# Performance work log

Measured on AMD Instinct MI355X. Metric: run time of the kernel, lower is better.

## Reference

```python
import jax, jax.numpy as jnp
import numpy as np
import math

B, C, H, W = 4, 64, 64, 64
N_HEAD = 1
GROUPS = 16
EPS = 1e-5


def dwconv_block(x, w, b, pad):
    # ReflectionPad2d(pad) -> depthwise Conv2d -> LeakyReLU(0.01)
    xp = jnp.pad(x, ((0, 0), (0, 0), (pad, pad), (pad, pad)), mode='reflect')
    y = jax.lax.conv_general_dilated(
        xp, w, window_strides=(1, 1), padding='VALID',
        dimension_numbers=('NCHW', 'OIHW', 'NCHW'),
        feature_group_count=x.shape[1])
    y = y + b[None, :, None, None]
    return jax.nn.leaky_relu(y, 0.01)


def group_norm(x, w, b):
    bb, c, h, ww = x.shape
    xg = x.reshape(bb, GROUPS, c // GROUPS, h, ww)
    mu = xg.mean(axis=(2, 3, 4), keepdims=True)
    var = xg.var(axis=(2, 3, 4), keepdims=True)
    xg = (xg - mu) * jax.lax.rsqrt(var + EPS)
    return xg.reshape(bb, c, h, ww) * w[None, :, None, None] + b[None, :, None, None]


def attention(q, k, v):
    # q,k,v: [B, n_head, head_dim, H, W]; softmax over flattened key grid
    bb, n, d, h, ww = q.shape
    qf = q.reshape(bb, n, d, h * ww)
    kf = k.reshape(bb, n, d, h * ww)
    vf = v.reshape(bb, n, d, h * ww)
    scores = jnp.einsum('bndq,bndk->bnqk', qf, kf) / math.sqrt(C)
    attn = jax.nn.softmax(scores, axis=-1)  # [B,n,HW,HW]
    out = jnp.einsum('bnqk,bndk->bndq', attn, vf)
    return out.reshape(bb, n * d, h, ww)


def conv1x1(x, w, b=None):
    y = jnp.einsum('oc,bchw->bohw', w, x)
    if b is not None:
        y = y + b[None, :, None, None]
    return y


def setup_inputs() -> dict:
    key = jax.random.key(0)
    ks = jax.random.split(key, 16)
    s = lambda fan: 1.0 / math.sqrt(fan)
    return {
        'inputs': jax.random.normal(ks[0], (B, C, H, W), jnp.float32),
        'dw1_w': jax.random.normal(ks[1], (C, 1, 3, 3), jnp.float32) * s(9),
        'dw1_b': jnp.zeros((C,), jnp.float32),
        'dw2_w': jax.random.normal(ks[2], (C, 1, 5, 5), jnp.float32) * s(25),
        'dw2_b': jnp.zeros((C,), jnp.float32),
        'gnA_w': jnp.ones((C,), jnp.float32),
        'gnA_b': jnp.zeros((C,), jnp.float32),
        'gnB_w': jnp.ones((C,), jnp.float32),
        'gnB_b': jnp.zeros((C,), jnp.float32),
        'qkvA_w': jax.random.normal(ks[3], (3 * C, C), jnp.float32) * s(C),
        'qkvB_w': jax.random.normal(ks[4], (3 * C, C), jnp.float32) * s(C),
        'outA_w': jax.random.normal(ks[5], (C, C), jnp.float32) * s(C),
        'outA_b': jnp.zeros((C,), jnp.float32),
        'outB_w': jax.random.normal(ks[6], (C, C), jnp.float32) * s(C),
        'outB_b': jnp.zeros((C,), jnp.float32),
    }


def reference(inputs, dw1_w, dw1_b, dw2_w, dw2_b, gnA_w, gnA_b, gnB_w, gnB_b,
              qkvA_w, qkvB_w, outA_w, outA_b, outB_w, outB_b):
    x = dwconv_block(inputs, dw1_w, dw1_b, pad=1)
    y = dwconv_block(inputs, dw2_w, dw2_b, pad=2)
    head_dim = C // N_HEAD

    x_A = group_norm(x, gnA_w, gnA_b)
    qkv_A = conv1x1(x_A, qkvA_w).reshape(B, N_HEAD, head_dim * 3, H, W)
    qA, kA, vA = jnp.split(qkv_A, 3, axis=2)

    x_B = group_norm(y, gnB_w, gnB_b)
    qkv_B = conv1x1(x_B, qkvB_w).reshape(B, N_HEAD, head_dim * 3, H, W)
    qB, kB, vB = jnp.split(qkv_B, 3, axis=2)

    # branch A: queries from B, keys/values from A
    out_A = conv1x1(attention(qB, kA, vA), outA_w, outA_b) + x_A
    # branch B: queries from A, keys/values from B
    out_B = conv1x1(attention(qA, kB, vB), outB_w, outB_b) + x_B
    return jnp.concatenate((out_A, out_B), axis=1)
```

## Files before the change

### kernel.cpp

```cpp
#include <hip/hip_runtime.h>
#include <hip/hip_bf16.h>

#define HW 4096
#define CCH 64

typedef __attribute__((ext_vector_type(8))) short short8;
typedef __attribute__((ext_vector_type(4))) float f32x4;
typedef unsigned short ushort_t;
typedef unsigned long long u64;

#define SCALE_Q 0.18033688f

__device__ __forceinline__ unsigned short f2b(float f) {
  unsigned u = __float_as_uint(f);
  return (unsigned short)((u + 0x7fff + ((u >> 16) & 1)) >> 16);
}
__device__ __forceinline__ float b2f(ushort_t u) {
  return __uint_as_float(((unsigned)u) << 16);
}
__device__ __forceinline__ unsigned cvtpk(float lo, float hi) {
  unsigned r;
  asm volatile("v_cvt_pk_bf16_f32 %0, %1, %2" : "=v"(r) : "v"(lo), "v"(hi));
  return r;
}
__device__ __forceinline__ void gload16(const void* g, void* l) {
  __builtin_amdgcn_global_load_lds(
      (const __attribute__((address_space(1))) unsigned int*)g,
      (__attribute__((address_space(3))) unsigned int*)l, 16, 0, 0);
}

__global__ void __launch_bounds__(256) k_dwconv(
    const float* __restrict__ in, const float* __restrict__ w1, const float* __restrict__ b1,
    const float* __restrict__ w2, const float* __restrict__ b2,
    ushort_t* __restrict__ x, ushort_t* __restrict__ y, float* __restrict__ sums) {
  __shared__ float sm[20 * 68];
  __shared__ float red[4][4];
  const int bc = blockIdx.x >> 2;
  const int r0 = (blockIdx.x & 3) * 16;
  const int c = bc & 63;
  const float* p = in + bc * HW;
  const int tid = threadIdx.x;
  for (int idx = tid; idx < 20 * 68; idx += 256) {
    int r = r0 + idx / 68 - 2, cc = idx % 68 - 2;
    r = r < 0 ? -r : (r > 63 ? 126 - r : r);
    cc = cc < 0 ? -cc : (cc > 63 ? 126 - cc : cc);
    sm[idx] = p[r * 64 + cc];
  }
  float w1r[9], w2r[25];
  for (int i = 0; i < 9; i++) w1r[i] = w1[c * 9 + i];
  for (int i = 0; i < 25; i++) w2r[i] = w2[c * 25 + i];
  const float bb1 = b1[c], bb2 = b2[c];
  __syncthreads();

  const int i = tid >> 4;
  const int j0 = (tid & 15) * 4;
  float rv[5][8];
  for (int u = 0; u < 5; u++) {
    *(f32x4*)&rv[u][0] = *(const f32x4*)&sm[(i + u) * 68 + j0];
    *(f32x4*)&rv[u][4] = *(const f32x4*)&sm[(i + u) * 68 + j0 + 4];
  }
  float a1[4], a2[4];
  for (int px = 0; px < 4; px++) {
    float s2 = bb2;
    for (int u = 0; u < 5; u++)
      for (int v = 0; v < 5; v++) s2 += w2r[u * 5 + v] * rv[u][px + v];
    float s1 = bb1;
    for (int u = 0; u < 3; u++)
      for (int v = 0; v < 3; v++) s1 += w1r[u * 3 + v] * rv[u + 1][px + 1 + v];
    a1[px] = s1 > 0.f ? s1 : 0.01f * s1;
    a2[px] = s2 > 0.f ? s2 : 0.01f * s2;
  }
  ushort_t t1[4], t2[4];
  for (int px = 0; px < 4; px++) { t1[px] = f2b(a1[px]); t2[px] = f2b(a2[px]); }
  const int off = bc * HW + (r0 + i) * 64 + j0;
  *(u64*)(x + off) = *(const u64*)t1;
  *(u64*)(y + off) = *(const u64*)t2;

  float s1 = 0, q1 = 0, s2 = 0, q2 = 0;
  for (int px = 0; px < 4; px++) {
    s1 += a1[px]; q1 += a1[px] * a1[px];
    s2 += a2[px]; q2 += a2[px] * a2[px];
  }
  for (int o = 1; o < 64; o <<= 1) {
    s1 += __shfl_xor(s1, o); q1 += __shfl_xor(q1, o);
    s2 += __shfl_xor(s2, o); q2 += __shfl_xor(q2, o);
  }
  if ((tid & 63) == 0) {
    red[tid >> 6][0] = s1; red[tid >> 6][1] = q1;
    red[tid >> 6][2] = s2; red[tid >> 6][3] = q2;
  }
  __syncthreads();
  if (tid == 0) {
    float r4[4];
    for (int k = 0; k < 4; k++)
      r4[k] = red[0][k] + red[1][k] + red[2][k] + red[3][k];
    const int b = bc >> 6, g = (bc & 63) >> 2;
    const int base = b * 32 + g * 2;
    atomicAdd(&sums[base], r4[0]);       atomicAdd(&sums[base + 1], r4[1]);
    atomicAdd(&sums[128 + base], r4[2]); atomicAdd(&sums[128 + base + 1], r4[3]);
  }
}

__global__ void __launch_bounds__(256) k_qkv(
    const ushort_t* __restrict__ xbf, const ushort_t* __restrict__ ybf,
    const float* __restrict__ sums,
    const float* __restrict__ gwA, const float* __restrict__ gbA,
    const float* __restrict__ gwB, const float* __restrict__ gbB,
    const float* __restrict__ wA, const float* __restrict__ wB,
    ushort_t* __restrict__ Qt, ushort_t* __restrict__ Kt, ushort_t* __restrict__ Vv) {
  __shared__ float scs[64], shs[64];
  const int id = blockIdx.x * 256 + threadIdx.x;
  const int pg = id & 1023;
  const int chunk = (id >> 10) % 24;
  const int h = id / (1024 * 24);
  const int b = h >> 1, br = h & 1;
  if (threadIdx.x < 64) {
    const int ch = threadIdx.x, g = ch >> 2;
    const float s = sums[br * 128 + b * 32 + g * 2];
    const float ss = sums[br * 128 + b * 32 + g * 2 + 1];
    const float mu = s * (1.f / 16384.f);
    const float var = ss * (1.f / 16384.f) - mu * mu;
    const float rsig = rsqrtf(var + 1e-5f);
    const float a = rsig * (br ? gwB : gwA)[ch];
    scs[ch] = a;
    shs[ch] = (br ? gbB : gbA)[ch] - mu * a;
  }
  __syncthreads();
  const ushort_t* X = (br ? ybf : xbf) + b * (CCH * HW);
  const float* W = br ? wB : wA;
  const int pix0 = pg * 4;
  const int r0 = chunk * 8;
  float acc[8][4];
  for (int r = 0; r < 8; r++) for (int p = 0; p < 4; p++) acc[r][p] = 0.f;
  for (int cc = 0; cc < 64; cc++) {
    const float sc = scs[cc], sh = shs[cc];
    const u64 raw = *(const u64*)(X + cc * HW + pix0);
    f32x4 xv;
    for (int p = 0; p < 4; p++)
      xv[p] = b2f((ushort_t)(raw >> (16 * p))) * sc + sh;
    for (int r = 0; r < 8; r++) {
      float wv = W[(r0 + r) * 64 + cc];
      for (int p = 0; p < 4; p++) acc[r][p] += wv * xv[p];
    }
  }
  if (chunk < 16) {
    ushort_t* dst = chunk < 8 ? Qt : Kt;
    const float qs = chunk < 8 ? SCALE_Q : 1.0f;
    const int d0 = (chunk & 7) * 8;
    for (int p = 0; p < 4; p++) {
      short8 v;
      for (int r = 0; r < 8; r++) v[r] = (short)f2b(acc[r][p] * qs);
      *(short8*)(dst + ((h * HW + pix0 + p) << 6) + d0) = v;
    }
  } else {
    const int d0 = (chunk - 16) * 8;
    for (int r = 0; r < 8; r++) {
      ushort_t tmp[4];
      for (int p = 0; p < 4; p++) tmp[p] = f2b(acc[r][p]);
      *(u64*)(Vv + (h * CCH + d0 + r) * HW + pix0) = *(const u64*)tmp;
    }
  }
}

__global__ void __launch_bounds__(256, 2) k_attn(
    const ushort_t* __restrict__ Qt, const ushort_t* __restrict__ Kt,
    const ushort_t* __restrict__ Vv,
    const float* __restrict__ oAw, const float* __restrict__ oAb,
    const float* __restrict__ oBw, const float* __restrict__ oBb,
    const ushort_t* __restrict__ xbf, const ushort_t* __restrict__ ybf,
    const float* __restrict__ sums,
    const float* __restrict__ gwA, const float* __restrict__ gbA,
    const float* __restrict__ gwB, const float* __restrict__ gbB,
    float* __restrict__ out) {
  __shared__ __align__(16) char lds[74240];
  const int h = blockIdx.x >> 6;
  const int qt = blockIdx.x & 63;
  const int b = h >> 1, br = h & 1;
  const int qh = b * 2 + (1 - br);
  const int tid = threadIdx.x;
  const int lane = tid & 63;
  const int wave = tid >> 6;
  const int q = lane & 15, g = lane >> 4;
  const int qbase = qt * 64 + wave * 16;

  float* scs = (float*)(lds + 73728);
  float* shs = scs + 64;
  if (tid < 64) {
    const int ch = tid, gg = ch >> 2;
    const float s = sums[br * 128 + b * 32 + gg * 2];
    const float ss = sums[br * 128 + b * 32 + gg * 2 + 1];
    const float mu = s * (1.f / 16384.f);
    const float var = ss * (1.f / 16384.f) - mu * mu;
    const float rsig = rsqrtf(var + 1e-5f);
    const float a = rsig * (br ? gwB : gwA)[ch];
    scs[ch] = a;
    shs[ch] = (br ? gbB : gbA)[ch] - mu * a;
  }

  const ushort_t* Qp = Qt + ((qh * HW + qbase + q) << 6);
  const short8 qf0 = *(const short8*)(Qp + g * 8);
  const short8 qf1 = *(const short8*)(Qp + 32 + g * 8);

  const ushort_t* Kh = Kt + ((u64)h * HW << 6);
  const ushort_t* Vh = Vv + (u64)h * (CCH * HW);
  const ushort_t* gk[4];
  const ushort_t* gv[4];
  for (int j = 0; j < 4; j++) {
    const int idx = j * 256 + tid;
    const int rK = idx >> 3, cK = (idx & 7) ^ (rK & 7);
    gk[j] = Kh + (rK << 6) + (cK << 3);
    const int rV = idx >> 4, cV = (idx & 15) ^ (rV & 7);
    gv[j] = Vh + rV * HW + (cV << 3);
  }
  char* lK = lds + (tid << 4);
  char* lV = lds + 16384 + (tid << 4);

  float m_run = -1e30f;
  f32x4 o[4] = {};
  f32x4 accl = {};
  char* wp = lds + 65536 + wave * 2048 + (q << 7);
  const int sw = (q & 7) << 4;
  short8 ones;
  for (int j = 0; j < 8; j++) ones[j] = (short)0x3F80;

  for (int j = 0; j < 4; j++) gload16(gk[j], lK + j * 4096);
  for (int j = 0; j < 4; j++) gload16(gv[j], lV + j * 4096);

#pragma unroll 1
  for (int it = 0; it < 32; ++it) {
    if (it < 31) {
      const int nb = (it + 1) & 1;
      for (int j = 0; j < 4; j++) gload16(gk[j] + (it + 1) * 8192, lK + nb * 32768 + j * 4096);
      for (int j = 0; j < 4; j++) gload16(gv[j] + (it + 1) * 128, lV + nb * 32768 + j * 4096);
      asm volatile("s_waitcnt vmcnt(8)" ::: "memory");
    } else {
      asm volatile("s_waitcnt vmcnt(0)" ::: "memory");
    }
    __builtin_amdgcn_s_barrier();

    const char* kb = lds + (it & 1) * 32768;
    const char* vb = kb + 16384;
#pragma unroll
    for (int ph = 0; ph < 2; ph++) {
      short8 ka[4][2], va[4][2];
      for (int c = 0; c < 4; c++)
        for (int s = 0; s < 2; s++)
          ka[c][s] = *(const short8*)(kb + ((ph * 64 + c * 16 + q) << 7) +
                                      (((s * 4 + g) ^ (q & 7)) << 4));
      for (int cd = 0; cd < 4; cd++)
        for (int s = 0; s < 2; s++)
          va[cd][s] = *(const short8*)(vb + ((cd * 16 + q) << 8) +
                                       (((ph * 8 + s * 4 + g) ^ (q & 7)) << 4));

      f32x4 sa[4];
      for (int c = 0; c < 4; c++) {
        f32x4 zz = {0.f, 0.f, 0.f, 0.f};
        zz = __builtin_amdgcn_mfma_f32_16x16x32_bf16(ka[c][0], qf0, zz, 0, 0, 0);
        sa[c] = __builtin_amdgcn_mfma_f32_16x16x32_bf16(ka[c][1], qf1, zz, 0, 0, 0);
      }
      float m0 = fmaxf(fmaxf(fmaxf(sa[0][0], sa[0][1]), sa[0][2]), sa[0][3]);
      float m1 = fmaxf(fmaxf(fmaxf(sa[1][0], sa[1][1]), sa[1][2]), sa[1][3]);
      float m2 = fmaxf(fmaxf(fmaxf(sa[2][0], sa[2][1]), sa[2][2]), sa[2][3]);
      float m3 = fmaxf(fmaxf(fmaxf(sa[3][0], sa[3][1]), sa[3][2]), sa[3][3]);
      float mloc = fmaxf(fmaxf(m0, m1), fmaxf(m2, m3));
      mloc = fmaxf(mloc, __shfl_xor(mloc, 16));
      mloc = fmaxf(mloc, __shfl_xor(mloc, 32));
      if (!__all(mloc <= m_run + 8.f)) {
        const float mnew = fmaxf(m_run, mloc);
        const float alpha = exp2f(m_run - mnew);
        for (int cd = 0; cd < 4; cd++)
          for (int i = 0; i < 4; i++) o[cd][i] *= alpha;
        for (int i = 0; i < 4; i++) accl[i] *= alpha;
        m_run = mnew;
      }
      u64 pk[4];
      for (int c = 0; c < 4; c++) {
        float p0 = exp2f(sa[c][0] - m_run), p1 = exp2f(sa[c][1] - m_run);
        float p2 = exp2f(sa[c][2] - m_run), p3 = exp2f(sa[c][3] - m_run);
        pk[c] = (u64)cvtpk(p0, p1) | ((u64)cvtpk(p2, p3) << 32);
      }
      for (int c = 0; c < 4; c++)
        *(u64*)(wp + (((c << 5) | (g << 3)) ^ sw)) = pk[c];
      asm volatile("s_waitcnt lgkmcnt(0)" ::: "memory");
      __builtin_amdgcn_sched_barrier(0);
      const short8 pb0 = *(const short8*)(wp + ((g << 4) ^ sw));
      const short8 pb1 = *(const short8*)(wp + ((64 | (g << 4)) ^ sw));
      for (int cd = 0; cd < 4; cd++) {
        o[cd] = __builtin_amdgcn_mfma_f32_16x16x32_bf16(va[cd][0], pb0, o[cd], 0, 0, 0);
        o[cd] = __builtin_amdgcn_mfma_f32_16x16x32_bf16(va[cd][1], pb1, o[cd], 0, 0, 0);
      }
      accl = __builtin_amdgcn_mfma_f32_16x16x32_bf16(ones, pb0, accl, 0, 0, 0);
      accl = __builtin_amdgcn_mfma_f32_16x16x32_bf16(ones, pb1, accl, 0, 0, 0);
    }
    __builtin_amdgcn_s_barrier();
  }

  __syncthreads();
  float* smW = (float*)(lds + wave * 4096);
  const float inv = 1.f / accl[0];
  for (int cd = 0; cd < 4; cd++) {
    f32x4 v;
    for (int i = 0; i < 4; i++) v[i] = o[cd][i] * inv;
    *(f32x4*)(smW + q * 64 + (((cd * 4 + g) ^ q) << 2)) = v;
  }
  asm volatile("s_waitcnt lgkmcnt(0)" ::: "memory");
  __builtin_amdgcn_sched_barrier(0);

  const float* W    = br ? oBw : oAw;
  const float* bias = br ? oBb : oAb;
  const ushort_t* xR = (br ? ybf : xbf) + b * (CCH * HW);
  const int q2 = lane & 15, g2 = lane >> 4;
  const float* smR = (float*)(lds + wave * 4096) + q2 * 64;
  const int pix = qt * 64 + wave * 16 + q2;

  float acc[16];
  for (int oi = 0; oi < 16; oi++) acc[oi] = bias[g2 * 16 + oi];
  for (int c4 = 0; c4 < 16; c4++) {
    const f32x4 Lv = *(const f32x4*)(smR + ((c4 ^ q2) << 2));
    for (int oi = 0; oi < 16; oi++) {
      const f32x4 wv = *(const f32x4*)(W + (g2 * 16 + oi) * 64 + c4 * 4);
      acc[oi] += wv[0] * Lv[0] + wv[1] * Lv[1] + wv[2] * Lv[2] + wv[3] * Lv[3];
    }
  }
  for (int oi = 0; oi < 16; oi++) {
    const int ch = g2 * 16 + oi;
    const float xn = b2f(xR[ch * HW + pix]) * scs[ch] + shs[ch];
    out[(b * 128 + br * 64 + ch) * HW + pix] = acc[oi] + xn;
  }
}

extern "C" void kernel_launch(void* const* d_in, const int* in_sizes, int n_in,
                              void* d_out, int out_size, void* d_ws, size_t ws_size,
                              hipStream_t stream) {
  const float* in   = (const float*)d_in[0];
  const float* dw1w = (const float*)d_in[1];
  const float* dw1b = (const float*)d_in[2];
  const float* dw2w = (const float*)d_in[3];
  const float* dw2b = (const float*)d_in[4];
  const float* gnAw = (const float*)d_in[5];
  const float* gnAb = (const float*)d_in[6];
  const float* gnBw = (const float*)d_in[7];
  const float* gnBb = (const float*)d_in[8];
  const float* qAw  = (const float*)d_in[9];
  const float* qBw  = (const float*)d_in[10];
  const float* oAw  = (const float*)d_in[11];
  const float* oAb  = (const float*)d_in[12];
  const float* oBw  = (const float*)d_in[13];
  const float* oBb  = (const float*)d_in[14];
  float* out = (float*)d_out;

  char* ws = (char*)d_ws;
  ushort_t* xbf = (ushort_t*)ws;
  ushort_t* ybf = xbf + 1048576;
  ushort_t* Qt  = ybf + 1048576;
  ushort_t* Kt  = Qt + 2097152;
  ushort_t* Vv  = Kt + 2097152;
  float* sums   = (float*)(Vv + 2097152);

  hipMemsetAsync(sums, 0, 256 * sizeof(float), stream);
  k_dwconv<<<1024, 256, 0, stream>>>(in, dw1w, dw1b, dw2w, dw2b, xbf, ybf, sums);
  k_qkv<<<768, 256, 0, stream>>>(xbf, ybf, sums, gnAw, gnAb, gnBw, gnBb,
                                 qAw, qBw, Qt, Kt, Vv);
  k_attn<<<512, 256, 0, stream>>>(Qt, Kt, Vv, oAw, oAb, oBw, oBb,
                                  xbf, ybf, sums, gnAw, gnAb, gnBw, gnBb, out);
}
```

Measured before the change: 224.7 us.

## Halve attention KV tile for 3 blocks/CU and drop atomic GN stats memset

The attention kernel's K/V tile shrinks from 128 to 64 keys per iteration, which halves the double-buffered LDS footprint and raises launch bounds to allow three blocks per CU. The inner loop runs 64 iterations with one phase each instead of 32 with two. Group-norm partial sums are now written per (channel, strip) with plain stores instead of atomics, and reduced with shuffles in the consumers, which removes the hipMemsetAsync launch. The trade-off is more barriers and loop overhead per key processed, plus register pressure under the tighter launch bound.

Result: faster. 219.8 us (-2.2%).

```diff
diff --git a/kernel.cpp b/kernel.cpp
--- a/kernel.cpp
+++ b/kernel.cpp
@@ -36,7 +36,8 @@
   __shared__ float sm[20 * 68];
   __shared__ float red[4][4];
   const int bc = blockIdx.x >> 2;
-  const int r0 = (blockIdx.x & 3) * 16;
+  const int strip = blockIdx.x & 3;
+  const int r0 = strip * 16;
   const int c = bc & 63;
   const float* p = in + bc * HW;
   const int tid = threadIdx.x;
@@ -94,11 +95,30 @@
     float r4[4];
     for (int k = 0; k < 4; k++)
       r4[k] = red[0][k] + red[1][k] + red[2][k] + red[3][k];
-    const int b = bc >> 6, g = (bc & 63) >> 2;
-    const int base = b * 32 + g * 2;
-    atomicAdd(&sums[base], r4[0]);       atomicAdd(&sums[base + 1], r4[1]);
-    atomicAdd(&sums[128 + base], r4[2]); atomicAdd(&sums[128 + base + 1], r4[3]);
-  }
+    sums[bc * 8 + strip * 2 + 0] = r4[0];
+    sums[bc * 8 + strip * 2 + 1] = r4[1];
+    sums[2048 + bc * 8 + strip * 2 + 0] = r4[2];
+    sums[2048 + bc * 8 + strip * 2 + 1] = r4[3];
+  }
+}
+
+__device__ __forceinline__ void gn_coeffs(
+    const float* __restrict__ sums, int b, int br, int ch,
+    const float* __restrict__ gw, const float* __restrict__ gb,
+    float& sc_out, float& sh_out) {
+  const float* pp = sums + br * 2048 + (b * 64 + ch) * 8;
+  const f32x4 pa = *(const f32x4*)pp;
+  const f32x4 pb = *(const f32x4*)(pp + 4);
+  float s = pa[0] + pa[2] + pb[0] + pb[2];
+  float ss = pa[1] + pa[3] + pb[1] + pb[3];
+  s += __shfl_xor(s, 1); ss += __shfl_xor(ss, 1);
+  s += __shfl_xor(s, 2); ss += __shfl_xor(ss, 2);
+  const float mu = s * (1.f / 16384.f);
+  const float var = ss * (1.f / 16384.f) - mu * mu;
+  const float rsig = rsqrtf(var + 1e-5f);
+  const float a = rsig * gw[ch];
+  sc_out = a;
+  sh_out = gb[ch] - mu * a;
 }
 
 __global__ void __launch_bounds__(256) k_qkv(
@@ -115,15 +135,10 @@
   const int h = id / (1024 * 24);
   const int b = h >> 1, br = h & 1;
   if (threadIdx.x < 64) {
-    const int ch = threadIdx.x, g = ch >> 2;
-    const float s = sums[br * 128 + b * 32 + g * 2];
-    const float ss = sums[br * 128 + b * 32 + g * 2 + 1];
-    const float mu = s * (1.f / 16384.f);
-    const float var = ss * (1.f / 16384.f) - mu * mu;
-    const float rsig = rsqrtf(var + 1e-5f);
-    const float a = rsig * (br ? gwB : gwA)[ch];
-    scs[ch] = a;
-    shs[ch] = (br ? gbB : gbA)[ch] - mu * a;
+    float a, sh;
+    gn_coeffs(sums, b, br, threadIdx.x, br ? gwB : gwA, br ? gbB : gbA, a, sh);
+    scs[threadIdx.x] = a;
+    shs[threadIdx.x] = sh;
   }
   __syncthreads();
   const ushort_t* X = (br ? ybf : xbf) + b * (CCH * HW);
@@ -162,7 +177,7 @@
   }
 }
 
-__global__ void __launch_bounds__(256, 2) k_attn(
+__global__ void __launch_bounds__(256, 3) k_attn(
     const ushort_t* __restrict__ Qt, const ushort_t* __restrict__ Kt,
     const ushort_t* __restrict__ Vv,
     const float* __restrict__ oAw, const float* __restrict__ oAb,
@@ -172,7 +187,7 @@
     const float* __restrict__ gwA, const float* __restrict__ gbA,
     const float* __restrict__ gwB, const float* __restrict__ gbB,
     float* __restrict__ out) {
-  __shared__ __align__(16) char lds[74240];
+  __shared__ __align__(16) char lds[41472];
   const int h = blockIdx.x >> 6;
   const int qt = blockIdx.x & 63;
   const int b = h >> 1, br = h & 1;
@@ -183,18 +198,13 @@
   const int q = lane & 15, g = lane >> 4;
   const int qbase = qt * 64 + wave * 16;
 
-  float* scs = (float*)(lds + 73728);
+  float* scs = (float*)(lds + 40960);
   float* shs = scs + 64;
   if (tid < 64) {
-    const int ch = tid, gg = ch >> 2;
-    const float s = sums[br * 128 + b * 32 + gg * 2];
-    const float ss = sums[br * 128 + b * 32 + gg * 2 + 1];
-    const float mu = s * (1.f / 16384.f);
-    const float var = ss * (1.f / 16384.f) - mu * mu;
-    const float rsig = rsqrtf(var + 1e-5f);
-    const float a = rsig * (br ? gwB : gwA)[ch];
-    scs[ch] = a;
-    shs[ch] = (br ? gbB : gbA)[ch] - mu * a;
+    float a, sh;
+    gn_coeffs(sums, b, br, tid, br ? gwB : gwA, br ? gbB : gbA, a, sh);
+    scs[tid] = a;
+    shs[tid] = sh;
   }
 
   const ushort_t* Qp = Qt + ((qh * HW + qbase + q) << 6);
@@ -203,95 +213,93 @@
 
   const ushort_t* Kh = Kt + ((u64)h * HW << 6);
   const ushort_t* Vh = Vv + (u64)h * (CCH * HW);
-  const ushort_t* gk[4];
-  const ushort_t* gv[4];
-  for (int j = 0; j < 4; j++) {
+  const ushort_t* gk[2];
+  const ushort_t* gv[2];
+  for (int j = 0; j < 2; j++) {
     const int idx = j * 256 + tid;
-    const int rK = idx >> 3, cK = (idx & 7) ^ (rK & 7);
-    gk[j] = Kh + (rK << 6) + (cK << 3);
-    const int rV = idx >> 4, cV = (idx & 15) ^ (rV & 7);
-    gv[j] = Vh + rV * HW + (cV << 3);
+    const int rr = idx >> 3, cc = (idx & 7) ^ (rr & 7);
+    gk[j] = Kh + (rr << 6) + (cc << 3);
+    gv[j] = Vh + rr * HW + (cc << 3);
   }
   char* lK = lds + (tid << 4);
-  char* lV = lds + 16384 + (tid << 4);
+  char* lV = lds + 8192 + (tid << 4);
 
   float m_run = -1e30f;
   f32x4 o[4] = {};
   f32x4 accl = {};
-  char* wp = lds + 65536 + wave * 2048 + (q << 7);
+  char* wp = lds + 32768 + wave * 2048 + (q << 7);
   const int sw = (q & 7) << 4;
   short8 ones;
   for (int j = 0; j < 8; j++) ones[j] = (short)0x3F80;
 
-  for (int j = 0; j < 4; j++) gload16(gk[j], lK + j * 4096);
-  for (int j = 0; j < 4; j++) gload16(gv[j], lV + j * 4096);
+  for (int j = 0; j < 2; j++) gload16(gk[j], lK + j * 4096);
+  for (int j = 0; j < 2; j++) gload16(gv[j], lV + j * 4096);
 
 #pragma unroll 1
-  for (int it = 0; it < 32; ++it) {
-    if (it < 31) {
+  for (int it = 0; it < 64; ++it) {
+    if (it < 63) {
       const int nb = (it + 1) & 1;
-      for (int j = 0; j < 4; j++) gload16(gk[j] + (it + 1) * 8192, lK + nb * 32768 + j * 4096);
-      for (int j = 0; j < 4; j++) gload16(gv[j] + (it + 1) * 128, lV + nb * 32768 + j * 4096);
-      asm volatile("s_waitcnt vmcnt(8)" ::: "memory");
+      for (int j = 0; j < 2; j++)
+        gload16(gk[j] + (it + 1) * 4096, lK + nb * 16384 + j * 4096);
+      for (int j = 0; j < 2; j++)
+        gload16(gv[j] + (it + 1) * 64, lV + nb * 16384 + j * 4096);
+      asm volatile("s_waitcnt vmcnt(4)" ::: "memory");
     } else {
       asm volatile("s_waitcnt vmcnt(0)" ::: "memory");
     }
     __builtin_amdgcn_s_barrier();
 
-    const char* kb = lds + (it & 1) * 32768;
-    const char* vb = kb + 16384;
-#pragma unroll
-    for (int ph = 0; ph < 2; ph++) {
-      short8 ka[4][2], va[4][2];
-      for (int c = 0; c < 4; c++)
-        for (int s = 0; s < 2; s++)
-          ka[c][s] = *(const short8*)(kb + ((ph * 64 + c * 16 + q) << 7) +
-                                      (((s * 4 + g) ^ (q & 7)) << 4));
+    const char* kb = lds + (it & 1) * 16384;
+    const char* vb = kb + 8192;
+    short8 ka[4][2], va[4][2];
+    for (int c = 0; c < 4; c++)
+      for (int s = 0; s < 2; s++)
+        ka[c][s] = *(const short8*)(kb + ((c * 16 + q) << 7) +
+                                    (((s * 4 + g) ^ (q & 7)) << 4));
+    for (int cd = 0; cd < 4; cd++)
+      for (int s = 0; s < 2; s++)
+        va[cd][s] = *(const short8*)(vb + ((cd * 16 + q) << 7) +
+                                     (((s * 4 + g) ^ (q & 7)) << 4));
+
+    f32x4 sa[4];
+    for (int c = 0; c < 4; c++) {
+      f32x4 zz = {0.f, 0.f, 0.f, 0.f};
+      zz = __builtin_amdgcn_mfma_f32_16x16x32_bf16(ka[c][0], qf0, zz, 0, 0, 0);
+      sa[c] = __builtin_amdgcn_mfma_f32_16x16x32_bf16(ka[c][1], qf1, zz, 0, 0, 0);
+    }
+    float m0 = fmaxf(fmaxf(fmaxf(sa[0][0], sa[0][1]), sa[0][2]), sa[0][3]);
+    float m1 = fmaxf(fmaxf(fmaxf(sa[1][0], sa[1][1]), sa[1][2]), sa[1][3]);
+    float m2 = fmaxf(fmaxf(fmaxf(sa[2][0], sa[2][1]), sa[2][2]), sa[2][3]);
+    float m3 = fmaxf(fmaxf(fmaxf(sa[3][0], sa[3][1]), sa[3][2]), sa[3][3]);
+    float mloc = fmaxf(fmaxf(m0, m1), fmaxf(m2, m3));
+    mloc = fmaxf(mloc, __shfl_xor(mloc, 16));
+    mloc = fmaxf(mloc, __shfl_xor(mloc, 32));
+    if (!__all(mloc <= m_run + 8.f)) {
+      const float mnew = fmaxf(m_run, mloc);
+      const float alpha = exp2f(m_run - mnew);
       for (int cd = 0; cd < 4; cd++)
-        for (int s = 0; s < 2; s++)
-          va[cd][s] = *(const short8*)(vb + ((cd * 16 + q) << 8) +
-                                       (((ph * 8 + s * 4 + g) ^ (q & 7)) << 4));
-
-      f32x4 sa[4];
-      for (int c = 0; c < 4; c++) {
-        f32x4 zz = {0.f, 0.f, 0.f, 0.f};
-        zz = __builtin_amdgcn_mfma_f32_16x16x32_bf16(ka[c][0], qf0, zz, 0, 0, 0);
-        sa[c] = __builtin_amdgcn_mfma_f32_16x16x32_bf16(ka[c][1], qf1, zz, 0, 0, 0);
-      }
-      float m0 = fmaxf(fmaxf(fmaxf(sa[0][0], sa[0][1]), sa[0][2]), sa[0][3]);
-      float m1 = fmaxf(fmaxf(fmaxf(sa[1][0], sa[1][1]), sa[1][2]), sa[1][3]);
-      float m2 = fmaxf(fmaxf(fmaxf(sa[2][0], sa[2][1]), sa[2][2]), sa[2][3]);
-      float m3 = fmaxf(fmaxf(fmaxf(sa[3][0], sa[3][1]), sa[3][2]), sa[3][3]);
-      float mloc = fmaxf(fmaxf(m0, m1), fmaxf(m2, m3));
-      mloc = fmaxf(mloc, __shfl_xor(mloc, 16));
-      mloc = fmaxf(mloc, __shfl_xor(mloc, 32));
-      if (!__all(mloc <= m_run + 8.f)) {
-        const float mnew = fmaxf(m_run, mloc);
-        const float alpha = exp2f(m_run - mnew);
-        for (int cd = 0; cd < 4; cd++)
-          for (int i = 0; i < 4; i++) o[cd][i] *= alpha;
-        for (int i = 0; i < 4; i++) accl[i] *= alpha;
-        m_run = mnew;
-      }
-      u64 pk[4];
-      for (int c = 0; c < 4; c++) {
-        float p0 = exp2f(sa[c][0] - m_run), p1 = exp2f(sa[c][1] - m_run);
-        float p2 = exp2f(sa[c][2] - m_run), p3 = exp2f(sa[c][3] - m_run);
-        pk[c] = (u64)cvtpk(p0, p1) | ((u64)cvtpk(p2, p3) << 32);
-      }
-      for (int c = 0; c < 4; c++)
-        *(u64*)(wp + (((c << 5) | (g << 3)) ^ sw)) = pk[c];
-      asm volatile("s_waitcnt lgkmcnt(0)" ::: "memory");
-      __builtin_amdgcn_sched_barrier(0);
-      const short8 pb0 = *(const short8*)(wp + ((g << 4) ^ sw));
-      const short8 pb1 = *(const short8*)(wp + ((64 | (g << 4)) ^ sw));
-      for (int cd = 0; cd < 4; cd++) {
-        o[cd] = __builtin_amdgcn_mfma_f32_16x16x32_bf16(va[cd][0], pb0, o[cd], 0, 0, 0);
-        o[cd] = __builtin_amdgcn_mfma_f32_16x16x32_bf16(va[cd][1], pb1, o[cd], 0, 0, 0);
-      }
-      accl = __builtin_amdgcn_mfma_f32_16x16x32_bf16(ones, pb0, accl, 0, 0, 0);
-      accl = __builtin_amdgcn_mfma_f32_16x16x32_bf16(ones, pb1, accl, 0, 0, 0);
-    }
+        for (int i = 0; i < 4; i++) o[cd][i] *= alpha;
+      for (int i = 0; i < 4; i++) accl[i] *= alpha;
+      m_run = mnew;
+    }
+    u64 pk[4];
+    for (int c = 0; c < 4; c++) {
+      float p0 = exp2f(sa[c][0] - m_run), p1 = exp2f(sa[c][1] - m_run);
+      float p2 = exp2f(sa[c][2] - m_run), p3 = exp2f(sa[c][3] - m_run);
+      pk[c] = (u64)cvtpk(p0, p1) | ((u64)cvtpk(p2, p3) << 32);
+    }
+    for (int c = 0; c < 4; c++)
+      *(u64*)(wp + (((c << 5) | (g << 3)) ^ sw)) = pk[c];
+    asm volatile("s_waitcnt lgkmcnt(0)" ::: "memory");
+    __builtin_amdgcn_sched_barrier(0);
+    const short8 pb0 = *(const short8*)(wp + ((g << 4) ^ sw));
+    const short8 pb1 = *(const short8*)(wp + ((64 | (g << 4)) ^ sw));
+    for (int cd = 0; cd < 4; cd++) {
+      o[cd] = __builtin_amdgcn_mfma_f32_16x16x32_bf16(va[cd][0], pb0, o[cd], 0, 0, 0);
+      o[cd] = __builtin_amdgcn_mfma_f32_16x16x32_bf16(va[cd][1], pb1, o[cd], 0, 0, 0);
+    }
+    accl = __builtin_amdgcn_mfma_f32_16x16x32_bf16(ones, pb0, accl, 0, 0, 0);
+    accl = __builtin_amdgcn_mfma_f32_16x16x32_bf16(ones, pb1, accl, 0, 0, 0);
     __builtin_amdgcn_s_barrier();
   }
 
@@ -357,7 +365,6 @@
   ushort_t* Vv  = Kt + 2097152;
   float* sums   = (float*)(Vv + 2097152);
 
-  hipMemsetAsync(sums, 0, 256 * sizeof(float), stream);
   k_dwconv<<<1024, 256, 0, stream>>>(in, dw1w, dw1b, dw2w, dw2b, xbf, ybf, sums);
   k_qkv<<<768, 256, 0, stream>>>(xbf, ybf, sums, gnAw, gnAb, gnBw, gnBb,
                                  qAw, qBw, Qt, Kt, Vv);
```
